# Kernel tuning notes

Hardware: AMD Instinct MI355X
Metric: run time of the kernel (lower is better)

Reference implementation:

```python
import jax, jax.numpy as jnp
import numpy as np

EPS = 1e-8

def setup_inputs() -> dict:
    key = jax.random.key(0)
    kq, kk, kv = jax.random.split(key, 3)
    S, B, D = 2048, 8, 64
    return {
        "query": jax.random.normal(kq, (S, B, D), dtype=jnp.float32),
        "key": jax.random.normal(kk, (S, B, D), dtype=jnp.float32),
        "value": jax.random.normal(kv, (S, B, D), dtype=jnp.float32),
    }

def reference(query, key, value):
    # SWAP-test fidelity: expval(Z) = |<q_hat|k_hat>|^2, overlap = 0.5*(1+Z).
    # Zero-padding to 2**n_qubits does not change the inner product.
    q_hat = query / (jnp.linalg.norm(query, axis=-1, keepdims=True) + EPS)
    k_hat = key / (jnp.linalg.norm(key, axis=-1, keepdims=True) + EPS)
    # cosine similarity per batch: [B, S_q, S_k]
    cos = jnp.einsum('ibd,jbd->bij', q_hat, k_hat)
    overlap = 0.5 * (1.0 + cos * cos)
    attn_probs = jax.nn.softmax(overlap, axis=-1)          # [B, S, S]
    context = jnp.einsum('bij,jbd->ibd', attn_probs, value)  # [S, B, D]
    attn_weights = jnp.transpose(attn_probs, (1, 0, 2))      # [S, B, S]
    return context, attn_weights
```

## Files before the change

kernel.cpp:

```cpp
#include <hip/hip_runtime.h>

#define S_LEN 2048
#define BATCH 8
#define DIM   64
#define QT    32
#define KTILE 128
#define NT2   16
#define NQT   128
#define PP    132
#define PBP   136
#define EPSV  1e-8f

#define WS_K_OFF (1u << 20)
#define WS_V_OFF (1u << 21)
#define WS_NEED_BYTES (6u * 1024u * 1024u)

typedef __attribute__((ext_vector_type(8))) short short8;
typedef __attribute__((ext_vector_type(4))) short short4v;
typedef __attribute__((ext_vector_type(4))) float f32x4;

__device__ __forceinline__ short bf16b(float x) {
    unsigned int u = __builtin_bit_cast(unsigned int, x);
    u = (u + 0x7fffu + ((u >> 16) & 1u)) >> 16;
    return (short)u;
}

#define LDS_BARRIER() do { \
    asm volatile("s_waitcnt lgkmcnt(0)" ::: "memory"); \
    __builtin_amdgcn_sched_barrier(0); \
    __builtin_amdgcn_s_barrier(); \
    __builtin_amdgcn_sched_barrier(0); \
} while (0)

__global__ __launch_bounds__(256)
void prep(const float* __restrict__ Qg, const float* __restrict__ Kg,
          const float* __restrict__ Vg, short* __restrict__ ws)
{
    const int blk = blockIdx.x;
    const int tid = threadIdx.x;
    if (blk < 512) {
        const bool isK = blk >= 256;
        const float* src = isK ? Kg : Qg;
        short* dst = ws + (isK ? WS_K_OFF : 0u);
        const int rg = (blk & 255) * 64 + (tid >> 2);
        const int rq = tid & 3;
        const int s = rg >> 3, b = rg & 7;
        const float4* rp = reinterpret_cast<const float4*>(src) + (size_t)rg * 16;
        float4 v[4];
        float ss = 0.f;
        #pragma unroll
        for (int c = 0; c < 4; ++c) {
            v[c] = rp[rq * 4 + c];
            ss += v[c].x*v[c].x + v[c].y*v[c].y + v[c].z*v[c].z + v[c].w*v[c].w;
        }
        ss += __shfl_xor(ss, 1);
        ss += __shfl_xor(ss, 2);
        const float sc = 1.f / (sqrtf(ss) + EPSV);
        const float* pf = reinterpret_cast<const float*>(v);
        #pragma unroll
        for (int h = 0; h < 2; ++h) {
            const int c8 = rq * 2 + h;
            const int kk = c8 >> 2, lg = c8 & 3;
            const int chunk = (b * NQT + (s >> 4)) * 128 + kk * 64 + lg * 16 + (s & 15);
            short8 o;
            #pragma unroll
            for (int j = 0; j < 8; ++j) o[j] = bf16b(pf[h * 8 + j] * sc);
            *reinterpret_cast<short8*>(dst + (size_t)chunk * 8) = o;
        }
    } else {
        const int cid = (blk - 512) * 256 + tid;
        const int l  = cid & 63;
        const int kk = (cid >> 6) & 1;
        const int gd = (cid >> 7) & 3;
        const int t  = (cid >> 9) & 31;
        const int b  = cid >> 14;
        const int d  = gd * 16 + (l & 15);
        const int k0 = t * 64 + kk * 32 + (l >> 4) * 8;
        short8 o;
        #pragma unroll
        for (int j = 0; j < 8; ++j)
            o[j] = bf16b(Vg[((size_t)(k0 + j) * BATCH + b) * DIM + d]);
        *reinterpret_cast<short8*>(ws + WS_V_OFF + (size_t)cid * 8) = o;
    }
}

__global__ __launch_bounds__(512, 4)
void qattn3(const short* __restrict__ Qp, const short* __restrict__ Kp,
            const short* __restrict__ Vp, float* __restrict__ out)
{
    __shared__ float Pf[QT * PP];
    __shared__ short Pb[QT * PBP];
    __shared__ float rsum[QT];

    const int tid = threadIdx.x;
    const int l   = tid & 63;
    const int w   = tid >> 6;
    const int lg  = l >> 4;
    const int lr  = l & 15;
    const int kg  = w;
    const int ms  = (w >> 2) * 16;
    const int dg  = w & 3;

    const int b     = blockIdx.x & 7;
    const int qt    = blockIdx.x >> 3;
    const int qbase = qt * QT;

    const short8* Qp8 = reinterpret_cast<const short8*>(Qp);
    short8 aq[2][2];
    #pragma unroll
    for (int m = 0; m < 2; ++m) {
        const size_t base = (size_t)(b * NQT + qt * 2 + m) * 128;
        aq[m][0] = Qp8[base + l];
        aq[m][1] = Qp8[base + 64 + l];
    }

    if (tid < QT) rsum[tid] = 0.f;
    __syncthreads();

    const short8* Kb8 = reinterpret_cast<const short8*>(Kp) + (size_t)b * NQT * 128;
    const short8* Vb8 = reinterpret_cast<const short8*>(Vp) + (size_t)b * 32 * 4 * 128;

    float sums[2][4] = {{0.f,0.f,0.f,0.f},{0.f,0.f,0.f,0.f}};
    short8 k0 = Kb8[(size_t)kg * 128 + l];
    short8 k1 = Kb8[(size_t)kg * 128 + 64 + l];
    for (int t = 0; t < NT2; ++t) {
        const int tn = (t + 1 < NT2) ? t + 1 : t;
        const short8* kc = &Kb8[(size_t)(8 * tn + kg) * 128 + l];
        const short8 kn0 = kc[0];
        const short8 kn1 = kc[64];
        #pragma unroll
        for (int m = 0; m < 2; ++m) {
            f32x4 acc = {0.f, 0.f, 0.f, 0.f};
            acc = __builtin_amdgcn_mfma_f32_16x16x32_bf16(aq[m][0], k0, acc, 0, 0, 0);
            acc = __builtin_amdgcn_mfma_f32_16x16x32_bf16(aq[m][1], k1, acc, 0, 0, 0);
            #pragma unroll
            for (int r = 0; r < 4; ++r) {
                float c = acc[r];
                sums[m][r] += __expf(0.5f + 0.5f * c * c);
            }
        }
        k0 = kn0; k1 = kn1;
    }
    #pragma unroll
    for (int m = 0; m < 2; ++m)
    #pragma unroll
    for (int r = 0; r < 4; ++r) {
        float v = sums[m][r];
        v += __shfl_xor(v, 1);
        v += __shfl_xor(v, 2);
        v += __shfl_xor(v, 4);
        v += __shfl_xor(v, 8);
        sums[m][r] = v;
    }
    if (lr == 0) {
        #pragma unroll
        for (int m = 0; m < 2; ++m)
        #pragma unroll
        for (int r = 0; r < 4; ++r)
            atomicAdd(&rsum[m * 16 + lg * 4 + r], sums[m][r]);
    }
    __syncthreads();
    float inv_[2][4];
    #pragma unroll
    for (int m = 0; m < 2; ++m)
    #pragma unroll
    for (int r = 0; r < 4; ++r)
        inv_[m][r] = 1.f / rsum[m * 16 + lg * 4 + r];

    float* attn = out + (size_t)S_LEN * BATCH * DIM;
    f32x4 cacc = {0.f, 0.f, 0.f, 0.f};

    k0 = Kb8[(size_t)kg * 128 + l];
    k1 = Kb8[(size_t)kg * 128 + 64 + l];

    for (int t = 0; t < NT2; ++t) {
        short8 bv[4];
        #pragma unroll
        for (int kk2 = 0; kk2 < 4; ++kk2) {
            const int tv = t * 2 + (kk2 >> 1);
            bv[kk2] = Vb8[(size_t)(tv * 4 + dg) * 128 + (kk2 & 1) * 64 + l];
        }
        const int tn = (t + 1 < NT2) ? t + 1 : t;
        const short8* kc = &Kb8[(size_t)(8 * tn + kg) * 128 + l];
        const short8 kn0 = kc[0];
        const short8 kn1 = kc[64];

        #pragma unroll
        for (int m = 0; m < 2; ++m) {
            f32x4 acc = {0.f, 0.f, 0.f, 0.f};
            acc = __builtin_amdgcn_mfma_f32_16x16x32_bf16(aq[m][0], k0, acc, 0, 0, 0);
            acc = __builtin_amdgcn_mfma_f32_16x16x32_bf16(aq[m][1], k1, acc, 0, 0, 0);
            #pragma unroll
            for (int r = 0; r < 4; ++r) {
                float c = acc[r];
                float p = __expf(0.5f + 0.5f * c * c) * inv_[m][r];
                const int q_r = m * 16 + lg * 4 + r;
                const int k_c = kg * 16 + lr;
                Pf[q_r * PP + k_c] = p;
                Pb[q_r * PBP + k_c] = bf16b(p);
            }
        }
        LDS_BARRIER();

        {
            const int q = tid >> 4;
            const int c = (tid & 15) * 4;
            f32x4 pv0 = *reinterpret_cast<const f32x4*>(&Pf[q * PP + c]);
            f32x4 pv1 = *reinterpret_cast<const f32x4*>(&Pf[q * PP + 64 + c]);
            float* dst = attn + (size_t)(qbase + q) * (BATCH * S_LEN) + b * S_LEN + t * KTILE;
            __builtin_nontemporal_store(pv0, reinterpret_cast<f32x4*>(dst + c));
            __builtin_nontemporal_store(pv1, reinterpret_cast<f32x4*>(dst + 64 + c));
        }

        #pragma unroll
        for (int kk2 = 0; kk2 < 4; ++kk2) {
            const short8 ap = *reinterpret_cast<const short8*>(
                &Pb[(ms + lr) * PBP + kk2 * 32 + lg * 8]);
            cacc = __builtin_amdgcn_mfma_f32_16x16x32_bf16(ap, bv[kk2], cacc, 0, 0, 0);
        }
        LDS_BARRIER();

        k0 = kn0; k1 = kn1;
    }

    #pragma unroll
    for (int r = 0; r < 4; ++r) {
        out[(size_t)(qbase + ms + lg * 4 + r) * (BATCH * DIM) + b * DIM + dg * 16 + lr]
            = cacc[r];
    }
}

#define FQT 32
#define FQP 72
#define FPP 68
#define FKT 64
#define FNT 32

__global__ __launch_bounds__(256, 4)
void qattn_fb(const float* __restrict__ Qg, const float* __restrict__ Kg,
              const float* __restrict__ Vg, float* __restrict__ out)
{
    __shared__ short Qsh[FQT * FQP];
    __shared__ short Ksh[FKT * FQP];
    __shared__ short VTs[DIM * FQP];
    __shared__ short Pb [FQT * FQP];
    __shared__ float Pf [FQT * FPP];
    __shared__ float rsum[FQT];

    const int tid = threadIdx.x;
    const int l   = tid & 63;
    const int w   = tid >> 6;
    const int lg  = l >> 4;
    const int lr  = l & 15;
    const int ms  = (w & 1) * 16;
    const int np  = (w >> 1) * 2;

    const int b     = blockIdx.x & 7;
    const int qtile = blockIdx.x >> 3;
    const int qbase = qtile * FQT;

    const int rr = tid >> 2;
    const int rq = tid & 3;

    if (tid < FQT * 4) {
        const float4* qp = reinterpret_cast<const float4*>(
            Qg + (size_t)(qbase + rr) * (BATCH * DIM) + b * DIM);
        float4 v[4];
        float ss = 0.f;
        #pragma unroll
        for (int c = 0; c < 4; ++c) {
            v[c] = qp[rq + 4 * c];
            ss += v[c].x*v[c].x + v[c].y*v[c].y + v[c].z*v[c].z + v[c].w*v[c].w;
        }
        ss += __shfl_xor(ss, 1);
        ss += __shfl_xor(ss, 2);
        const float sc = 1.f / (sqrtf(ss) + EPSV);
        #pragma unroll
        for (int c = 0; c < 4; ++c) {
            short4v s4 = { bf16b(v[c].x * sc), bf16b(v[c].y * sc),
                           bf16b(v[c].z * sc), bf16b(v[c].w * sc) };
            *reinterpret_cast<short4v*>(&Qsh[rr * FQP + rq * 4 + 16 * c]) = s4;
        }
    }
    if (tid < FQT) rsum[tid] = 0.f;
    __syncthreads();

    short8 aq[2];
    #pragma unroll
    for (int kk = 0; kk < 2; ++kk)
        aq[kk] = *reinterpret_cast<const short8*>(&Qsh[(ms + lr) * FQP + kk * 32 + lg * 8]);

    float sums[4] = {0.f, 0.f, 0.f, 0.f};
    for (int t = 0; t < FNT; ++t) {
        __syncthreads();
        {
            const float4* kp = reinterpret_cast<const float4*>(
                Kg + (size_t)(t * FKT + rr) * (BATCH * DIM) + b * DIM);
            float4 v[4];
            float ss = 0.f;
            #pragma unroll
            for (int c = 0; c < 4; ++c) {
                v[c] = kp[rq + 4 * c];
                ss += v[c].x*v[c].x + v[c].y*v[c].y + v[c].z*v[c].z + v[c].w*v[c].w;
            }
            ss += __shfl_xor(ss, 1);
            ss += __shfl_xor(ss, 2);
            const float sc = 1.f / (sqrtf(ss) + EPSV);
            #pragma unroll
            for (int c = 0; c < 4; ++c) {
                short4v s4 = { bf16b(v[c].x * sc), bf16b(v[c].y * sc),
                               bf16b(v[c].z * sc), bf16b(v[c].w * sc) };
                *reinterpret_cast<short4v*>(&Ksh[rr * FQP + rq * 4 + 16 * c]) = s4;
            }
        }
        __syncthreads();
        #pragma unroll
        for (int g = 0; g < 2; ++g) {
            f32x4 acc = {0.f, 0.f, 0.f, 0.f};
            #pragma unroll
            for (int kk = 0; kk < 2; ++kk) {
                short8 bk = *reinterpret_cast<const short8*>(
                    &Ksh[((np + g) * 16 + lr) * FQP + kk * 32 + lg * 8]);
                acc = __builtin_amdgcn_mfma_f32_16x16x32_bf16(aq[kk], bk, acc, 0, 0, 0);
            }
            #pragma unroll
            for (int r = 0; r < 4; ++r) {
                float c = acc[r];
                sums[r] += __expf(0.5f + 0.5f * c * c);
            }
        }
    }
    #pragma unroll
    for (int r = 0; r < 4; ++r) {
        float v = sums[r];
        v += __shfl_xor(v, 1);
        v += __shfl_xor(v, 2);
        v += __shfl_xor(v, 4);
        v += __shfl_xor(v, 8);
        sums[r] = v;
    }
    if (lr == 0) {
        #pragma unroll
        for (int r = 0; r < 4; ++r)
            atomicAdd(&rsum[ms + lg * 4 + r], sums[r]);
    }
    __syncthreads();
    float inv4[4];
    #pragma unroll
    for (int r = 0; r < 4; ++r)
        inv4[r] = 1.f / rsum[ms + lg * 4 + r];

    float* attn = out + (size_t)S_LEN * BATCH * DIM;
    f32x4 cacc[2];
    cacc[0] = (f32x4){0.f, 0.f, 0.f, 0.f};
    cacc[1] = (f32x4){0.f, 0.f, 0.f, 0.f};

    for (int t = 0; t < FNT; ++t) {
        __syncthreads();
        {
            const float4* kp = reinterpret_cast<const float4*>(
                Kg + (size_t)(t * FKT + rr) * (BATCH * DIM) + b * DIM);
            float4 v[4];
            float ss = 0.f;
            #pragma unroll
            for (int c = 0; c < 4; ++c) {
                v[c] = kp[rq + 4 * c];
                ss += v[c].x*v[c].x + v[c].y*v[c].y + v[c].z*v[c].z + v[c].w*v[c].w;
            }
            ss += __shfl_xor(ss, 1);
            ss += __shfl_xor(ss, 2);
            const float sc = 1.f / (sqrtf(ss) + EPSV);
            #pragma unroll
            for (int c = 0; c < 4; ++c) {
                short4v s4 = { bf16b(v[c].x * sc), bf16b(v[c].y * sc),
                               bf16b(v[c].z * sc), bf16b(v[c].w * sc) };
                *reinterpret_cast<short4v*>(&Ksh[rr * FQP + rq * 4 + 16 * c]) = s4;
            }
        }
        {
            const float4* vp = reinterpret_cast<const float4*>(
                Vg + (size_t)(t * FKT + rr) * (BATCH * DIM) + b * DIM);
            #pragma unroll
            for (int c = 0; c < 4; ++c) {
                float4 v = vp[rq + 4 * c];
                int d0 = rq * 4 + 16 * c;
                VTs[(d0 + 0) * FQP + rr] = bf16b(v.x);
                VTs[(d0 + 1) * FQP + rr] = bf16b(v.y);
                VTs[(d0 + 2) * FQP + rr] = bf16b(v.z);
                VTs[(d0 + 3) * FQP + rr] = bf16b(v.w);
            }
        }
        __syncthreads();
        #pragma unroll
        for (int g = 0; g < 2; ++g) {
            f32x4 acc = {0.f, 0.f, 0.f, 0.f};
            #pragma unroll
            for (int kk = 0; kk < 2; ++kk) {
                short8 bk = *reinterpret_cast<const short8*>(
                    &Ksh[((np + g) * 16 + lr) * FQP + kk * 32 + lg * 8]);
                acc = __builtin_amdgcn_mfma_f32_16x16x32_bf16(aq[kk], bk, acc, 0, 0, 0);
            }
            #pragma unroll
            for (int r = 0; r < 4; ++r) {
                float c = acc[r];
                float p = __expf(0.5f + 0.5f * c * c) * inv4[r];
                int q_r = ms + lg * 4 + r;
                int k_c = (np + g) * 16 + lr;
                Pf[q_r * FPP + k_c] = p;
                Pb[q_r * FQP + k_c] = bf16b(p);
            }
        }
        __syncthreads();
        #pragma unroll
        for (int g = 0; g < 2; ++g) {
            #pragma unroll
            for (int kk = 0; kk < 2; ++kk) {
                short8 ap = *reinterpret_cast<const short8*>(
                    &Pb[(ms + lr) * FQP + kk * 32 + lg * 8]);
                short8 bv = *reinterpret_cast<const short8*>(
                    &VTs[((np + g) * 16 + lr) * FQP + kk * 32 + lg * 8]);
                cacc[g] = __builtin_amdgcn_mfma_f32_16x16x32_bf16(ap, bv, cacc[g], 0, 0, 0);
            }
        }
        #pragma unroll
        for (int s = 0; s < 2; ++s) {
            int q  = s * 16 + (tid >> 4);
            int c4 = (tid & 15) * 4;
            f32x4 pv = *reinterpret_cast<const f32x4*>(&Pf[q * FPP + c4]);
            __builtin_nontemporal_store(pv, reinterpret_cast<f32x4*>(
                attn + (size_t)(qbase + q) * (BATCH * S_LEN) + b * S_LEN + t * FKT + c4));
        }
    }

    #pragma unroll
    for (int g = 0; g < 2; ++g) {
        #pragma unroll
        for (int r = 0; r < 4; ++r) {
            __builtin_nontemporal_store(cacc[g][r],
                out + (size_t)(qbase + ms + lg * 4 + r) * (BATCH * DIM)
                    + b * DIM + (np + g) * 16 + lr);
        }
    }
}

extern "C" void kernel_launch(void* const* d_in, const int* in_sizes, int n_in,
                              void* d_out, int out_size, void* d_ws, size_t ws_size,
                              hipStream_t stream)
{
    const float* q = (const float*)d_in[0];
    const float* k = (const float*)d_in[1];
    const float* v = (const float*)d_in[2];
    float* o  = (float*)d_out;

    if (ws_size >= WS_NEED_BYTES && d_ws != nullptr) {
        short* ws = (short*)d_ws;
        prep<<<1024, 256, 0, stream>>>(q, k, v, ws);
        qattn3<<<BATCH * (S_LEN / QT), 512, 0, stream>>>(ws, ws + WS_K_OFF, ws + WS_V_OFF, o);
    } else {
        qattn_fb<<<BATCH * (S_LEN / FQT), 256, 0, stream>>>(q, k, v, o);
    }
}
```

Before: 169.6 us.

## Cache unnormalized exp scores in LDS to skip second QK pass

The kernel stores the bf16 exponentiated scores for the whole key range in a large LDS buffer during the row-sum pass. It then writes normalized attention weights from that buffer and runs the PV MFMA from it, split across two key halves reduced through LDS. This removes the recomputation of QK and exp and the per-tile barriers. In exchange, LDS use grows to roughly 130KB, which cuts occupancy, and the attention weights are now emitted from bf16-rounded values instead of fp32.

Result: slower. 218.3 us (+28.7%).

```diff
diff --git a/kernel.cpp b/kernel.cpp
--- a/kernel.cpp
+++ b/kernel.cpp
@@ -4,11 +4,10 @@
 #define BATCH 8
 #define DIM   64
 #define QT    32
-#define KTILE 128
-#define NT2   16
+#define NTK   16
 #define NQT   128
-#define PP    132
-#define PBP   136
+#define PBP2  2056
+#define CTXP  68
 #define EPSV  1e-8f
 
 #define WS_K_OFF (1u << 20)
@@ -23,6 +22,10 @@
     unsigned int u = __builtin_bit_cast(unsigned int, x);
     u = (u + 0x7fffu + ((u >> 16) & 1u)) >> 16;
     return (short)u;
+}
+__device__ __forceinline__ float bf2f(short s) {
+    unsigned int u = ((unsigned int)(unsigned short)s) << 16;
+    return __builtin_bit_cast(float, u);
 }
 
 #define LDS_BARRIER() do { \
@@ -84,12 +87,11 @@
     }
 }
 
-__global__ __launch_bounds__(512, 4)
-void qattn3(const short* __restrict__ Qp, const short* __restrict__ Kp,
+__global__ __launch_bounds__(512, 2)
+void qattn4(const short* __restrict__ Qp, const short* __restrict__ Kp,
             const short* __restrict__ Vp, float* __restrict__ out)
 {
-    __shared__ float Pf[QT * PP];
-    __shared__ short Pb[QT * PBP];
+    __shared__ short Pbuf[QT * PBP2];
     __shared__ float rsum[QT];
 
     const int tid = threadIdx.x;
@@ -97,9 +99,6 @@
     const int w   = tid >> 6;
     const int lg  = l >> 4;
     const int lr  = l & 15;
-    const int kg  = w;
-    const int ms  = (w >> 2) * 16;
-    const int dg  = w & 3;
 
     const int b     = blockIdx.x & 7;
     const int qt    = blockIdx.x >> 3;
@@ -121,11 +120,11 @@
     const short8* Vb8 = reinterpret_cast<const short8*>(Vp) + (size_t)b * 32 * 4 * 128;
 
     float sums[2][4] = {{0.f,0.f,0.f,0.f},{0.f,0.f,0.f,0.f}};
-    short8 k0 = Kb8[(size_t)kg * 128 + l];
-    short8 k1 = Kb8[(size_t)kg * 128 + 64 + l];
-    for (int t = 0; t < NT2; ++t) {
-        const int tn = (t + 1 < NT2) ? t + 1 : t;
-        const short8* kc = &Kb8[(size_t)(8 * tn + kg) * 128 + l];
+    short8 k0 = Kb8[(size_t)w * 128 + l];
+    short8 k1 = Kb8[(size_t)w * 128 + 64 + l];
+    for (int t = 0; t < NTK; ++t) {
+        const int tn = (t + 1 < NTK) ? t + 1 : t;
+        const short8* kc = &Kb8[(size_t)(8 * tn + w) * 128 + l];
         const short8 kn0 = kc[0];
         const short8 kn1 = kc[64];
         #pragma unroll
@@ -135,8 +134,10 @@
             acc = __builtin_amdgcn_mfma_f32_16x16x32_bf16(aq[m][1], k1, acc, 0, 0, 0);
             #pragma unroll
             for (int r = 0; r < 4; ++r) {
-                float c = acc[r];
-                sums[m][r] += __expf(0.5f + 0.5f * c * c);
+                const float c = acc[r];
+                const float e = __expf(0.5f + 0.5f * c * c);
+                sums[m][r] += e;
+                Pbuf[(m * 16 + lg * 4 + r) * PBP2 + t * 128 + w * 16 + lr] = bf16b(e);
             }
         }
         k0 = kn0; k1 = kn1;
@@ -159,74 +160,72 @@
         for (int r = 0; r < 4; ++r)
             atomicAdd(&rsum[m * 16 + lg * 4 + r], sums[m][r]);
     }
-    __syncthreads();
-    float inv_[2][4];
+    LDS_BARRIER();
+
+    float* attn = out + (size_t)S_LEN * BATCH * DIM;
+    {
+        const int q   = tid >> 4;
+        const int l16 = tid & 15;
+        const float invq = 1.f / rsum[q];
+        float* dstrow = attn + (size_t)(qbase + q) * (BATCH * S_LEN) + b * S_LEN;
+        #pragma unroll 4
+        for (int it = 0; it < 16; ++it) {
+            const int cb = it * 128 + l16 * 8;
+            const short8 pv = *reinterpret_cast<const short8*>(&Pbuf[q * PBP2 + cb]);
+            f32x4 o0, o1;
+            #pragma unroll
+            for (int j = 0; j < 4; ++j) {
+                o0[j] = bf2f(pv[j])     * invq;
+                o1[j] = bf2f(pv[4 + j]) * invq;
+            }
+            __builtin_nontemporal_store(o0, reinterpret_cast<f32x4*>(dstrow + cb));
+            __builtin_nontemporal_store(o1, reinterpret_cast<f32x4*>(dstrow + cb + 4));
+        }
+    }
+
+    const int dg = w & 3;
+    const int kh = w >> 2;
+    f32x4 cacc[2];
+    cacc[0] = (f32x4){0.f, 0.f, 0.f, 0.f};
+    cacc[1] = (f32x4){0.f, 0.f, 0.f, 0.f};
+    for (int ks = 0; ks < 32; ++ks) {
+        const int t64 = kh * 16 + (ks >> 1);
+        const int kk  = ks & 1;
+        const short8 bv = Vb8[(size_t)(t64 * 4 + dg) * 128 + kk * 64 + l];
+        const int kb = kh * 1024 + ks * 32;
+        #pragma unroll
+        for (int m = 0; m < 2; ++m) {
+            const short8 ap = *reinterpret_cast<const short8*>(
+                &Pbuf[(m * 16 + lr) * PBP2 + kb + lg * 8]);
+            cacc[m] = __builtin_amdgcn_mfma_f32_16x16x32_bf16(ap, bv, cacc[m], 0, 0, 0);
+        }
+    }
+    float invr[2][4];
     #pragma unroll
     for (int m = 0; m < 2; ++m)
     #pragma unroll
     for (int r = 0; r < 4; ++r)
-        inv_[m][r] = 1.f / rsum[m * 16 + lg * 4 + r];
-
-    float* attn = out + (size_t)S_LEN * BATCH * DIM;
-    f32x4 cacc = {0.f, 0.f, 0.f, 0.f};
-
-    k0 = Kb8[(size_t)kg * 128 + l];
-    k1 = Kb8[(size_t)kg * 128 + 64 + l];
-
-    for (int t = 0; t < NT2; ++t) {
-        short8 bv[4];
-        #pragma unroll
-        for (int kk2 = 0; kk2 < 4; ++kk2) {
-            const int tv = t * 2 + (kk2 >> 1);
-            bv[kk2] = Vb8[(size_t)(tv * 4 + dg) * 128 + (kk2 & 1) * 64 + l];
-        }
-        const int tn = (t + 1 < NT2) ? t + 1 : t;
-        const short8* kc = &Kb8[(size_t)(8 * tn + kg) * 128 + l];
-        const short8 kn0 = kc[0];
-        const short8 kn1 = kc[64];
-
-        #pragma unroll
-        for (int m = 0; m < 2; ++m) {
-            f32x4 acc = {0.f, 0.f, 0.f, 0.f};
-            acc = __builtin_amdgcn_mfma_f32_16x16x32_bf16(aq[m][0], k0, acc, 0, 0, 0);
-            acc = __builtin_amdgcn_mfma_f32_16x16x32_bf16(aq[m][1], k1, acc, 0, 0, 0);
-            #pragma unroll
-            for (int r = 0; r < 4; ++r) {
-                float c = acc[r];
-                float p = __expf(0.5f + 0.5f * c * c) * inv_[m][r];
-                const int q_r = m * 16 + lg * 4 + r;
-                const int k_c = kg * 16 + lr;
-                Pf[q_r * PP + k_c] = p;
-                Pb[q_r * PBP + k_c] = bf16b(p);
-            }
-        }
-        LDS_BARRIER();
-
-        {
-            const int q = tid >> 4;
-            const int c = (tid & 15) * 4;
-            f32x4 pv0 = *reinterpret_cast<const f32x4*>(&Pf[q * PP + c]);
-            f32x4 pv1 = *reinterpret_cast<const f32x4*>(&Pf[q * PP + 64 + c]);
-            float* dst = attn + (size_t)(qbase + q) * (BATCH * S_LEN) + b * S_LEN + t * KTILE;
-            __builtin_nontemporal_store(pv0, reinterpret_cast<f32x4*>(dst + c));
-            __builtin_nontemporal_store(pv1, reinterpret_cast<f32x4*>(dst + 64 + c));
-        }
-
-        #pragma unroll
-        for (int kk2 = 0; kk2 < 4; ++kk2) {
-            const short8 ap = *reinterpret_cast<const short8*>(
-                &Pb[(ms + lr) * PBP + kk2 * 32 + lg * 8]);
-            cacc = __builtin_amdgcn_mfma_f32_16x16x32_bf16(ap, bv[kk2], cacc, 0, 0, 0);
-        }
-        LDS_BARRIER();
-
-        k0 = kn0; k1 = kn1;
-    }
-
-    #pragma unroll
-    for (int r = 0; r < 4; ++r) {
-        out[(size_t)(qbase + ms + lg * 4 + r) * (BATCH * DIM) + b * DIM + dg * 16 + lr]
-            = cacc[r];
+        invr[m][r] = 1.f / rsum[m * 16 + lg * 4 + r];
+
+    LDS_BARRIER();
+    float* ctxb = reinterpret_cast<float*>(Pbuf);
+    if (kh == 1) {
+        #pragma unroll
+        for (int m = 0; m < 2; ++m)
+        #pragma unroll
+        for (int r = 0; r < 4; ++r)
+            ctxb[(m * 16 + lg * 4 + r) * CTXP + dg * 16 + lr] = cacc[m][r];
+    }
+    LDS_BARRIER();
+    if (kh == 0) {
+        #pragma unroll
+        for (int m = 0; m < 2; ++m)
+        #pragma unroll
+        for (int r = 0; r < 4; ++r) {
+            const int row = m * 16 + lg * 4 + r;
+            const float v = (cacc[m][r] + ctxb[row * CTXP + dg * 16 + lr]) * invr[m][r];
+            out[(size_t)(qbase + row) * (BATCH * DIM) + b * DIM + dg * 16 + lr] = v;
+        }
     }
 }
 
@@ -455,7 +454,7 @@
     if (ws_size >= WS_NEED_BYTES && d_ws != nullptr) {
         short* ws = (short*)d_ws;
         prep<<<1024, 256, 0, stream>>>(q, k, v, ws);
-        qattn3<<<BATCH * (S_LEN / QT), 512, 0, stream>>>(ws, ws + WS_K_OFF, ws + WS_V_OFF, o);
+        qattn4<<<BATCH * (S_LEN / QT), 512, 0, stream>>>(ws, ws + WS_K_OFF, ws + WS_V_OFF, o);
     } else {
         qattn_fb<<<BATCH * (S_LEN / FQT), 256, 0, stream>>>(q, k, v, o);
     }
```
